# Performance work log

Measured on AMD Instinct MI355X. Metric: run time of the kernel, lower is better.

Reference implementation:

```python
import jax, jax.numpy as jnp
import numpy as np

B, L, D = 32, 512, 128          # batch, seq_len, d_model (= num graph nodes N)
E, HS, DTR, U = 64, 64, 4, 32   # d_proj_E, d_proj_H (state), dt_rank, d_proj_U
R, K, DE, NH = 3, 3, 10, 4      # mamba layers, cheb order, d_e, heads
EPS = 1e-5


def _ln(x, g, b):
    m = jnp.mean(x, -1, keepdims=True)
    v = jnp.mean((x - m) ** 2, -1, keepdims=True)
    return (x - m) / jnp.sqrt(v + EPS) * g + b


def _mamba(x, in_w, conv_w, conv_b, xproj_w, dt_w, dt_b, Alog, Dp, out_w):
    b, l, _ = x.shape
    xz = x @ in_w                                  # (b,l,2E)
    xp, res = xz[..., :E], xz[..., E:]
    xc = jnp.transpose(xp, (0, 2, 1))              # (b,E,l)
    # causal depthwise conv: torch pads both sides by d_conv-1 then slices [:l]
    xc = jax.lax.conv_general_dilated(
        xc, conv_w, (1,), [(conv_w.shape[-1] - 1, 0)],
        dimension_numbers=('NCH', 'OIH', 'NCH'), feature_group_count=E)
    xc = xc + conv_b[None, :, None]
    xp = jax.nn.silu(jnp.transpose(xc, (0, 2, 1)))  # (b,l,E)
    xdbl = xp @ xproj_w                             # (b,l,DTR+2*HS)
    delta = jax.nn.softplus(xdbl[..., :DTR] @ dt_w + dt_b)        # (b,l,E)
    Bm = xdbl[..., DTR:DTR + HS]                                   # (b,l,HS)
    Cm = xdbl[..., DTR + HS:]                                      # (b,l,HS)
    A = -jnp.exp(Alog)                                             # (E,HS)
    dA = jnp.exp(delta[..., None] * A)                             # (b,l,E,HS)
    dBu = delta[..., None] * Bm[:, :, None, :] * xp[..., None]     # (b,l,E,HS)

    def step(s, t):
        dA_t, dBu_t, C_t = t
        s = dA_t * s + dBu_t
        return s, jnp.einsum('bdn,bn->bd', s, C_t)

    _, ys = jax.lax.scan(step, jnp.zeros((b, E, HS), x.dtype),
                         (jnp.swapaxes(dA, 0, 1), jnp.swapaxes(dBu, 0, 1),
                          jnp.swapaxes(Cm, 0, 1)))
    y = jnp.swapaxes(ys, 0, 1) + xp * Dp
    y = y * jax.nn.sigmoid(res)
    return y @ out_w


def _forward(x, mb_in_w, mb_conv_w, mb_conv_b, mb_xproj_w, mb_dt_w, mb_dt_b,
             mb_Alog, mb_D, mb_out_w, ln1_g, ln1_b, ln2_g, ln2_b,
             ffn_w1, ffn_b1, ffn_w2, ffn_b2,
             psi_emb, psi, W_q, W_k, attn_alpha, F_w, f_b, head_mix,
             head_w, head_b):
    # ---- bidirectional Mamba stack ----
    for i in range(R):
        f, bk = 2 * i, 2 * i + 1
        Y1 = _mamba(x, mb_in_w[f], mb_conv_w[f], mb_conv_b[f], mb_xproj_w[f],
                    mb_dt_w[f], mb_dt_b[f], mb_Alog[f], mb_D[f], mb_out_w[f])
        Y2 = jnp.flip(_mamba(jnp.flip(x, 1), mb_in_w[bk], mb_conv_w[bk],
                             mb_conv_b[bk], mb_xproj_w[bk], mb_dt_w[bk],
                             mb_dt_b[bk], mb_Alog[bk], mb_D[bk], mb_out_w[bk]), 1)
        Y3 = _ln(x + Y1 + Y2, ln1_g[i], ln1_b[i])
        Yp = jax.nn.relu(Y3 @ ffn_w1[i] + ffn_b1[i]) @ ffn_w2[i] + ffn_b2[i]
        x = _ln(Yp + Y3, ln2_g[i], ln2_b[i])
    h = jnp.transpose(x, (0, 2, 1))                # (B, N=D, L)
    # ---- MAGAC (deterministic single MC sample, eval, no edge drop) ----
    diff = psi_emb[:, None, :] - psi_emb[None, :, :]
    A_g = jax.nn.softmax(jnp.exp(-psi * jnp.sum(diff * diff, -1)), axis=1)
    Q = jnp.einsum('nd,dhm->nhm', psi_emb, W_q)
    Kt = jnp.einsum('nd,dhm->nhm', psi_emb, W_k)
    attn = jax.nn.softmax(jnp.einsum('nhd,mhd->hnm', Q, Kt)
                          / jnp.sqrt(jnp.asarray(DE, x.dtype)), axis=-1)
    alpha = jax.nn.sigmoid(attn_alpha)
    A_effs = alpha * A_g[None] + (1.0 - alpha) * attn   # (H,N,N)
    mix = jax.nn.softmax(head_mix)
    I = jnp.eye(D, dtype=x.dtype)
    out = jnp.zeros((x.shape[0], D), x.dtype)
    for hh in range(NH):
        A = A_effs[hh]
        sup = [I, A]
        for _ in range(2, K + 1):
            sup.append(2.0 * A @ sup[-1] - sup[-2])
        S = jnp.stack(sup, 0)                             # (K+1,N,N)
        Wf = jnp.einsum('nd,dkl->nkl', psi_emb, F_w[hh])  # (N,K+1,L)
        bf = psi_emb @ f_b[hh]                            # (N,)
        out_h = jnp.einsum('knm,bml,nkl->bn', S, h, Wf) + bf
        out = out + mix[hh] * out_h
    log_var = jnp.zeros_like(out)
    pred = out @ head_w + head_b                          # (B,1)
    return pred, log_var


def setup_inputs() -> dict:
    key = jax.random.key(0)
    ks = iter(jax.random.split(key, 40))
    nrm = lambda shp, s=0.05: (jax.random.normal(next(ks), shp, jnp.float32) * s)
    M = 2 * R
    base_Alog = jnp.log(jnp.arange(1, HS + 1, dtype=jnp.float32))
    inp = {
        'x': jax.random.normal(next(ks), (B, L, D), jnp.float32),
        'mb_in_w': nrm((M, D, 2 * E)),
        'mb_conv_w': nrm((M, E, 1, 3), 0.2),
        'mb_conv_b': jnp.zeros((M, E), jnp.float32),
        'mb_xproj_w': nrm((M, E, DTR + 2 * HS)),
        'mb_dt_w': nrm((M, DTR, E), 0.2),
        'mb_dt_b': jnp.zeros((M, E), jnp.float32),
        'mb_Alog': jnp.tile(base_Alog[None, None, :], (M, E, 1)),
        'mb_D': jnp.ones((M, E), jnp.float32),
        'mb_out_w': nrm((M, E, D)),
        'ln1_g': jnp.ones((R, D), jnp.float32),
        'ln1_b': jnp.zeros((R, D), jnp.float32),
        'ln2_g': jnp.ones((R, D), jnp.float32),
        'ln2_b': jnp.zeros((R, D), jnp.float32),
        'ffn_w1': nrm((R, D, U)),
        'ffn_b1': jnp.zeros((R, U), jnp.float32),
        'ffn_w2': nrm((R, U, D)),
        'ffn_b2': jnp.zeros((R, D), jnp.float32),
        'psi_emb': jax.random.normal(next(ks), (D, DE), jnp.float32),
        'psi': jnp.asarray(1.0, jnp.float32),
        'W_q': jax.random.normal(next(ks), (DE, NH, DE), jnp.float32),
        'W_k': jax.random.normal(next(ks), (DE, NH, DE), jnp.float32),
        'attn_alpha': jnp.asarray(0.5, jnp.float32),
        'F_w': nrm((NH, DE, K + 1, L), 0.05),
        'f_b': nrm((NH, DE), 1.0),
        'head_mix': jnp.ones((NH,), jnp.float32),
        'head_w': nrm((D, 1)),
        'head_b': jnp.zeros((1,), jnp.float32),
    }
    return inp


def reference(x, mb_in_w, mb_conv_w, mb_conv_b, mb_xproj_w, mb_dt_w, mb_dt_b,
              mb_Alog, mb_D, mb_out_w, ln1_g, ln1_b, ln2_g, ln2_b,
              ffn_w1, ffn_b1, ffn_w2, ffn_b2,
              psi_emb, psi, W_q, W_k, attn_alpha, F_w, f_b, head_mix,
              head_w, head_b):
    return _forward(x, mb_in_w, mb_conv_w, mb_conv_b, mb_xproj_w, mb_dt_w,
                    mb_dt_b, mb_Alog, mb_D, mb_out_w, ln1_g, ln1_b, ln2_g,
                    ln2_b, ffn_w1, ffn_b1, ffn_w2, ffn_b2, psi_emb, psi,
                    W_q, W_k, attn_alpha, F_w, f_b, head_mix, head_w, head_b)
```

## Files before the change

### kernel.cpp

```cpp
#include <hip/hip_runtime.h>
#include <hip/hip_bf16.h>


#define B_ 32
#define L_ 512
#define D_ 128
#define E_ 64
#define HS_ 64

#define OFF_X     0u
#define OFF_XZF   2097152u
#define OFF_XZB   4194304u
#define OFF_XPF   6291456u
#define OFF_XPB   7340032u
#define OFF_PKF   8388608u
#define OFF_PKB   10485760u
#define OFF_XBCF  12582912u
#define OFF_XBCB  14680064u
#define OFF_YSF   16777216u
#define OFF_YSB   17825792u
#define OFF_V     2097152u
#define OFF_WFT   10485760u
#define OFF_STT   11534336u
#define OFF_AEFF  11796480u
#define OFF_PART  12582912u
#define OFF_RED1  16777216u

__device__ __forceinline__ float sigf(float x) { return 1.f / (1.f + __expf(-x)); }
__device__ __forceinline__ unsigned int bf16r(float x) {
    unsigned int u = __float_as_uint(x);
    return (u + 0x7fffu + ((u >> 16) & 1u)) >> 16;
}

__global__ __launch_bounds__(256) void gemm_in2_kernel(
    const float* __restrict__ X, const float* __restrict__ WF, const float* __restrict__ WB,
    float* __restrict__ xzF, float* __restrict__ xzB)
{
    __shared__ float sxT[128][36];
    __shared__ float sw[2][16][128];
    const int tid = threadIdx.x;
    const int r0 = blockIdx.x * 32;
    for (int q = tid; q < 1024; q += 256) {
        const int r = q >> 5, k4 = q & 31;
        const float4 v = *(const float4*)&X[(size_t)(r0 + r) * 128 + k4 * 4];
        sxT[k4 * 4 + 0][r] = v.x; sxT[k4 * 4 + 1][r] = v.y;
        sxT[k4 * 4 + 2][r] = v.z; sxT[k4 * 4 + 3][r] = v.w;
    }
    const int wv = tid >> 6, lane = tid & 63;
    const int d = wv >> 1, ch = wv & 1;
    const int r4 = lane >> 4, c16 = lane & 15;
    float4 acc[8];
#pragma unroll
    for (int j = 0; j < 8; ++j) acc[j] = float4{0.f, 0.f, 0.f, 0.f};
    for (int ko = 0; ko < 128; ko += 16) {
        __syncthreads();
        for (int q = tid; q < 1024; q += 256) {
            const int dd = q >> 9, kk = (q >> 5) & 15, c4 = q & 31;
            *(float4*)&sw[dd][kk][c4 * 4] =
                *(const float4*)&((dd ? WB : WF)[(ko + kk) * 128 + c4 * 4]);
        }
        __syncthreads();
#pragma unroll
        for (int kk = 0; kk < 16; ++kk) {
            const float4 w4 = *(const float4*)&sw[d][kk][ch * 64 + c16 * 4];
            const float4 xa = *(const float4*)&sxT[ko + kk][r4 * 8];
            const float4 xb = *(const float4*)&sxT[ko + kk][r4 * 8 + 4];
            const float xs[8] = {xa.x, xa.y, xa.z, xa.w, xb.x, xb.y, xb.z, xb.w};
#pragma unroll
            for (int j = 0; j < 8; ++j) {
                acc[j].x = fmaf(xs[j], w4.x, acc[j].x);
                acc[j].y = fmaf(xs[j], w4.y, acc[j].y);
                acc[j].z = fmaf(xs[j], w4.z, acc[j].z);
                acc[j].w = fmaf(xs[j], w4.w, acc[j].w);
            }
        }
    }
    float* xz = d ? xzB : xzF;
#pragma unroll
    for (int j = 0; j < 8; ++j) {
        *(float4*)&xz[(r0 + r4 * 8 + j) * 128 + ch * 64 + c16 * 4] = acc[j];
    }
}

__global__ __launch_bounds__(256) void prep4_kernel(
    const float* __restrict__ xzF_, const float* __restrict__ xzB_,
    const float* __restrict__ conv_w, const float* __restrict__ conv_b,
    const float* __restrict__ xproj_w, const float* __restrict__ dt_w,
    const float* __restrict__ dt_b, int layer,
    float* __restrict__ xpF_, float* __restrict__ xpB_,
    unsigned int* __restrict__ xbcF_, unsigned int* __restrict__ xbcB_,
    float* __restrict__ pkF_, float* __restrict__ pkB_)
{
    __shared__ float sW[8448];
    __shared__ float sxp4[4][64][4];
    __shared__ float sdl4[4][4][4];
    const int tid = threadIdx.x, wv = tid >> 6, lane = tid & 63;
    const int dir = (int)(blockIdx.x >= 1024);
    const int r0 = (blockIdx.x & 1023) * 16;
    const int b = r0 >> 9;
    const int m = layer * 2 + dir;
    const float* Wg = xproj_w + m * 8448;
    for (int q = tid; q < 2112; q += 256) ((float4*)sW)[q] = ((const float4*)Wg)[q];
    const float* xz = dir ? xzB_ : xzF_;
    float* xp  = dir ? xpB_  : xpF_;
    unsigned int* xbc = dir ? xbcB_ : xbcF_;
    float* pkx = dir ? pkB_  : pkF_;
    const float* cw = conv_w + m * 192 + lane * 3;
    const float cw0 = cw[0], cw1 = cw[1], cw2 = cw[2];
    const float cb  = conv_b[m * 64 + lane];
    const float dtb = dt_b[m * 64 + lane];
    const float* dwp = dt_w + m * 256;
    const float dw0 = dwp[lane], dw1 = dwp[64 + lane], dw2 = dwp[128 + lane], dw3 = dwp[192 + lane];
    float uu[4];
#pragma unroll
    for (int it = 0; it < 4; ++it) {
        const int row = r0 + wv * 4 + it;
        const int l = row & 511;
        const int l1 = dir ? l + 1 : l - 1;
        const int l2 = dir ? l + 2 : l - 2;
        float acc = cb;
        const float x0 = xz[(size_t)row * 128 + lane];
        const float x1 = (l1 >= 0 && l1 < 512) ? xz[(size_t)(b * 512 + l1) * 128 + lane] : 0.f;
        const float x2 = (l2 >= 0 && l2 < 512) ? xz[(size_t)(b * 512 + l2) * 128 + lane] : 0.f;
        acc += cw0 * x2 + cw1 * x1 + cw2 * x0;
        const float u = acc * sigf(acc);
        xp[row * 64 + lane] = u;
        uu[it] = u;
    }
    *(float4*)&sxp4[wv][lane][0] = float4{uu[0], uu[1], uu[2], uu[3]};
    __syncthreads();
    const int jdt = lane & 3;
    float aB[4] = {0.f, 0.f, 0.f, 0.f};
    float aC[4] = {0.f, 0.f, 0.f, 0.f};
    float adt[4] = {0.f, 0.f, 0.f, 0.f};
#pragma unroll 4
    for (int k = 0; k < 64; ++k) {
        const float wB = sW[k * 132 + 4 + lane];
        const float wC = sW[k * 132 + 68 + lane];
        const float wd = sW[k * 132 + jdt];
        const float4 xv = *(const float4*)&sxp4[wv][k][0];
        aB[0] = fmaf(xv.x, wB, aB[0]); aC[0] = fmaf(xv.x, wC, aC[0]); adt[0] = fmaf(xv.x, wd, adt[0]);
        aB[1] = fmaf(xv.y, wB, aB[1]); aC[1] = fmaf(xv.y, wC, aC[1]); adt[1] = fmaf(xv.y, wd, adt[1]);
        aB[2] = fmaf(xv.z, wB, aB[2]); aC[2] = fmaf(xv.z, wC, aC[2]); adt[2] = fmaf(xv.z, wd, adt[2]);
        aB[3] = fmaf(xv.w, wB, aB[3]); aC[3] = fmaf(xv.w, wC, aC[3]); adt[3] = fmaf(xv.w, wd, adt[3]);
    }
#pragma unroll
    for (int it = 0; it < 4; ++it) {
        const int row = r0 + wv * 4 + it;
        xbc[row * 64 + lane] = (bf16r(aC[it]) << 16) | bf16r(aB[it]);
        if (lane < 4) sdl4[wv][it][lane] = adt[it];
    }
#pragma unroll
    for (int it = 0; it < 4; ++it) {
        const int row = r0 + wv * 4 + it;
        float dpre = fmaf(sdl4[wv][it][0], dw0, dtb);
        dpre = fmaf(sdl4[wv][it][1], dw1, dpre);
        dpre = fmaf(sdl4[wv][it][2], dw2, dpre);
        dpre = fmaf(sdl4[wv][it][3], dw3, dpre);
        const float dlt = (dpre > 20.f) ? dpre : log1pf(__expf(dpre));
        ((float2*)pkx)[row * 64 + lane] = float2{dlt, dlt * uu[it]};
    }
}

__global__ __launch_bounds__(256, 4) void scan8_kernel(
    const unsigned int* __restrict__ xbcF, const unsigned int* __restrict__ xbcB,
    const float* __restrict__ pkF, const float* __restrict__ pkB,
    const float* __restrict__ AlogF, const float* __restrict__ AlogB,
    float* __restrict__ ysF, float* __restrict__ ysB)
{
    __shared__ unsigned int sbc[2][1024];
    __shared__ float spk[2][4][16][2];
    __shared__ float ytile[4][16][68];
    const int tid = threadIdx.x, wv = tid >> 6, lane = tid & 63;
    const int bx = blockIdx.x;
    const int db = bx & 63;
    const int dir = db >> 5;
    const int b   = db & 31;
    const int e0  = (bx >> 6) * 4;
    const int e   = e0 + wv;
    const unsigned int* xbc = dir ? xbcB : xbcF;
    const float* pk  = dir ? pkB  : pkF;
    const float* Aw  = dir ? AlogB : AlogF;
    float* ys = dir ? ysB : ysF;
    const float a2 = -__expf(Aw[e * 64 + lane]) * 1.4426950408889634f;
    float s = 0.f;
    float* yrow = ys + (size_t)(b * 64 + e) * 512;

    const int psl = tid & 15, pw_ = tid >> 4;

#define STG_LOAD(RS)                                                              \
    {                                                                             \
        nb = *(const uint4*)(xbc + (size_t)(RS) * 64 + tid * 4);                  \
        if (tid < 64)                                                             \
            npp = *(const float2*)(pk + (size_t)((RS) + psl) * 128 + (e0 + pw_) * 2); \
    }
#define STG_WRITE(BUF)                                                            \
    {                                                                             \
        *(uint4*)(&sbc[BUF][tid * 4]) = nb;                                       \
        if (tid < 64) *(float2*)(&spk[BUF][pw_][psl][0]) = npp;                   \
    }

#define SCAN16(REV)                                                               \
    {                                                                             \
        const unsigned int* bc = &sbc[cur][0];                                    \
        const float* pq = &spk[cur][wv][0][0];                                    \
        _Pragma("unroll")                                                         \
        for (int j = 0; j < 8; ++j) {                                             \
            const int pj = (REV) ? 7 - j : j;                                     \
            const float4 pk4 = *(const float4*)(pq + pj * 4);                     \
            const int sA = (REV) ? 15 - 2 * j : 2 * j;                            \
            const int sB = (REV) ? 14 - 2 * j : 2 * j + 1;                        \
            const float dlA = (REV) ? pk4.z : pk4.x;                              \
            const float duA = (REV) ? pk4.w : pk4.y;                              \
            const float dlB = (REV) ? pk4.x : pk4.z;                              \
            const float duB = (REV) ? pk4.y : pk4.w;                              \
            const unsigned int bA = bc[sA * 64 + lane];                           \
            const float BnA = __uint_as_float(bA << 16);                          \
            const float CnA = __uint_as_float(bA & 0xffff0000u);                  \
            s = fmaf(__builtin_amdgcn_exp2f(dlA * a2), s, duA * BnA);             \
            ytile[wv][sA][lane] = s * CnA;                                        \
            const unsigned int bB = bc[sB * 64 + lane];                           \
            const float BnB = __uint_as_float(bB << 16);                          \
            const float CnB = __uint_as_float(bB & 0xffff0000u);                  \
            s = fmaf(__builtin_amdgcn_exp2f(dlB * a2), s, duB * BnB);             \
            ytile[wv][sB][lane] = s * CnB;                                        \
        }                                                                         \
    }

    {
        uint4 nb; float2 npp;
        const int rs0 = b * 512 + (dir ? 496 : 0);
        STG_LOAD(rs0);
        STG_WRITE(0);
    }
    __syncthreads();

    int cur = 0;
    const int rr = lane & 15, sg = lane >> 4;
    for (int t = 0; t < 32; ++t) {
        uint4 nb; float2 npp;
        const bool more = (t + 1) < 32;
        if (more) {
            const int rs = b * 512 + (dir ? (496 - (t + 1) * 16) : ((t + 1) * 16));
            STG_LOAD(rs);
        }
        if (dir == 0) { SCAN16(0) } else { SCAN16(1) }
        {
            const float* yt = &ytile[wv][rr][sg * 16];
            const float4 A0 = *(const float4*)yt;
            const float4 A1 = *(const float4*)(yt + 4);
            const float4 A2 = *(const float4*)(yt + 8);
            const float4 A3 = *(const float4*)(yt + 12);
            float p = ((A0.x + A0.y) + (A0.z + A0.w)) + ((A1.x + A1.y) + (A1.z + A1.w))
                    + ((A2.x + A2.y) + (A2.z + A2.w)) + ((A3.x + A3.y) + (A3.z + A3.w));
            p += __shfl_xor(p, 16);
            p += __shfl_xor(p, 32);
            if (lane < 16) {
                const int lg = dir ? (496 + rr - t * 16) : (t * 16 + rr);
                yrow[lg] = p;
            }
        }
        if (more) STG_WRITE(cur ^ 1);
        __syncthreads();
        cur ^= 1;
    }
#undef STG_LOAD
#undef STG_WRITE
#undef SCAN16
}

__global__ __launch_bounds__(256, 4) void opfn3_kernel(
    const float* __restrict__ ysF, const float* __restrict__ ysB,
    const float* __restrict__ xpF, const float* __restrict__ xpB,
    const float* __restrict__ xzF, const float* __restrict__ xzB,
    const float* __restrict__ Dp, int layer,
    const float* __restrict__ Xc, const float* __restrict__ out_w,
    const float* __restrict__ W1, const float* __restrict__ b1,
    const float* __restrict__ W2, const float* __restrict__ b2,
    const float* __restrict__ g1, const float* __restrict__ bb1,
    const float* __restrict__ g2, const float* __restrict__ bb2,
    float* __restrict__ xout,
    const float* __restrict__ WFn, const float* __restrict__ WBn,
    float* __restrict__ xzFo, float* __restrict__ xzBo)
{
    __shared__ float smem[9216];
    float* syy = smem;
    float* sw  = smem + 4096;
    float* sh  = smem + 8192;
    const int tid = threadIdx.x;
    const int r0 = blockIdx.x * 32;
    const int b = r0 >> 9, l0 = r0 & 511;
    const int wv = tid >> 6, lane = tid & 63;
    const float* WFp = out_w + (layer * 2) * 8192;
    const float* WBp = out_w + (layer * 2 + 1) * 8192;

    for (int q = tid; q < 1024; q += 256) {
        const int d = q >> 9, ee = (q >> 3) & 63, rq = q & 7;
        const float* ysp = d ? ysB : ysF;
        const float4 v = *(const float4*)&ysp[(size_t)(b * 64 + ee) * 512 + l0 + rq * 4];
        const float dv = Dp[(layer * 2 + d) * 64 + ee];
        const float* xpp = d ? xpB : xpF;
        const float* xzp = d ? xzB : xzF;
        const float vv[4] = {v.x, v.y, v.z, v.w};
#pragma unroll
        for (int j = 0; j < 4; ++j) {
            const int r = rq * 4 + j;
            const int row = r0 + r;
            const float u   = xpp[(size_t)row * 64 + ee];
            const float res = xzp[(size_t)row * 128 + 64 + ee];
            syy[r * 128 + d * 64 + ee] = (vv[j] + u * dv) * sigf(res);
        }
    }
    __syncthreads();

    float acc[8][2];
#pragma unroll
    for (int r = 0; r < 8; ++r) { acc[r][0] = 0.f; acc[r][1] = 0.f; }
#define OPSTEP8(COMP, J)                                                          \
        {                                                                         \
            const float w0 = sw[(kk + (J)) * 128 + lane];                         \
            const float w1 = sw[(kk + (J)) * 128 + lane + 64];                    \
            acc[0][0] = fmaf(y40.COMP, w0, acc[0][0]); acc[0][1] = fmaf(y40.COMP, w1, acc[0][1]); \
            acc[1][0] = fmaf(y41.COMP, w0, acc[1][0]); acc[1][1] = fmaf(y41.COMP, w1, acc[1][1]); \
            acc[2][0] = fmaf(y42.COMP, w0, acc[2][0]); acc[2][1] = fmaf(y42.COMP, w1, acc[2][1]); \
            acc[3][0] = fmaf(y43.COMP, w0, acc[3][0]); acc[3][1] = fmaf(y43.COMP, w1, acc[3][1]); \
            acc[4][0] = fmaf(y44.COMP, w0, acc[4][0]); acc[4][1] = fmaf(y44.COMP, w1, acc[4][1]); \
            acc[5][0] = fmaf(y45.COMP, w0, acc[5][0]); acc[5][1] = fmaf(y45.COMP, w1, acc[5][1]); \
            acc[6][0] = fmaf(y46.COMP, w0, acc[6][0]); acc[6][1] = fmaf(y46.COMP, w1, acc[6][1]); \
            acc[7][0] = fmaf(y47.COMP, w0, acc[7][0]); acc[7][1] = fmaf(y47.COMP, w1, acc[7][1]); \
        }
#define GEMM_CHUNK8(SRC, KO)                                                      \
    _Pragma("unroll")                                                             \
    for (int kk = 0; kk < 32; kk += 4) {                                          \
        const float4 y40 = *(const float4*)&(SRC)[(wv * 8 + 0) * 128 + (KO) + kk];\
        const float4 y41 = *(const float4*)&(SRC)[(wv * 8 + 1) * 128 + (KO) + kk];\
        const float4 y42 = *(const float4*)&(SRC)[(wv * 8 + 2) * 128 + (KO) + kk];\
        const float4 y43 = *(const float4*)&(SRC)[(wv * 8 + 3) * 128 + (KO) + kk];\
        const float4 y44 = *(const float4*)&(SRC)[(wv * 8 + 4) * 128 + (KO) + kk];\
        const float4 y45 = *(const float4*)&(SRC)[(wv * 8 + 5) * 128 + (KO) + kk];\
        const float4 y46 = *(const float4*)&(SRC)[(wv * 8 + 6) * 128 + (KO) + kk];\
        const float4 y47 = *(const float4*)&(SRC)[(wv * 8 + 7) * 128 + (KO) + kk];\
        OPSTEP8(x, 0) OPSTEP8(y, 1) OPSTEP8(z, 2) OPSTEP8(w, 3)                  \
    }
    for (int koi = 0; koi < 4; ++koi) {
        if (koi) __syncthreads();
        for (int q = tid; q < 1024; q += 256) {
            const int kk = q >> 5, c4 = q & 31;
            const int kg = koi * 32 + kk;
            *(float4*)&sw[kk * 128 + c4 * 4] = (kg < 64)
                ? *(const float4*)&WFp[kg * 128 + c4 * 4]
                : *(const float4*)&WBp[(kg - 64) * 128 + c4 * 4];
        }
        __syncthreads();
        GEMM_CHUNK8(syy, koi * 32);
    }
    __syncthreads();
    for (int q = tid; q < 1024; q += 256) ((float4*)sw)[q] = ((const float4*)W1)[q];
#pragma unroll
    for (int r = 0; r < 8; ++r) {
        const int rl = wv * 8 + r;
        const int row = r0 + rl;
        float v0 = acc[r][0] + Xc[(size_t)row * 128 + lane];
        float v1 = acc[r][1] + Xc[(size_t)row * 128 + lane + 64];
        float sum = v0 + v1, sq = v0 * v0 + v1 * v1;
#pragma unroll
        for (int o = 32; o >= 1; o >>= 1) { sum += __shfl_xor(sum, o); sq += __shfl_xor(sq, o); }
        const float mean = sum * (1.f / 128.f);
        const float var = sq * (1.f / 128.f) - mean * mean;
        const float rs = rsqrtf(var + 1e-5f);
        syy[rl * 128 + lane]      = (v0 - mean) * rs * g1[lane] + bb1[lane];
        syy[rl * 128 + lane + 64] = (v1 - mean) * rs * g1[lane + 64] + bb1[lane + 64];
    }
    __syncthreads();
    {
        const int r = tid >> 3, ug = (tid & 7) * 4;
        float h0 = b1[ug], h1 = b1[ug + 1], h2 = b1[ug + 2], h3 = b1[ug + 3];
#pragma unroll 8
        for (int k = 0; k < 128; ++k) {
            const float xv = syy[r * 128 + k];
            h0 = fmaf(xv, sw[k * 32 + ug], h0);
            h1 = fmaf(xv, sw[k * 32 + ug + 1], h1);
            h2 = fmaf(xv, sw[k * 32 + ug + 2], h2);
            h3 = fmaf(xv, sw[k * 32 + ug + 3], h3);
        }
        sh[r * 32 + ug]     = fmaxf(h0, 0.f);
        sh[r * 32 + ug + 1] = fmaxf(h1, 0.f);
        sh[r * 32 + ug + 2] = fmaxf(h2, 0.f);
        sh[r * 32 + ug + 3] = fmaxf(h3, 0.f);
    }
    __syncthreads();
    for (int q = tid; q < 1024; q += 256) ((float4*)sw)[q] = ((const float4*)W2)[q];
    __syncthreads();
    float xr[8][2];
#pragma unroll
    for (int r = 0; r < 8; ++r) {
        const int rl = wv * 8 + r;
        float a0 = b2[lane], a1 = b2[lane + 64];
#pragma unroll 8
        for (int k = 0; k < 32; ++k) {
            const float hv = sh[rl * 32 + k];
            a0 = fmaf(hv, sw[k * 128 + lane], a0);
            a1 = fmaf(hv, sw[k * 128 + lane + 64], a1);
        }
        const float v0 = a0 + syy[rl * 128 + lane];
        const float v1 = a1 + syy[rl * 128 + lane + 64];
        float sum = v0 + v1, sq = v0 * v0 + v1 * v1;
#pragma unroll
        for (int o = 32; o >= 1; o >>= 1) { sum += __shfl_xor(sum, o); sq += __shfl_xor(sq, o); }
        const float mean = sum * (1.f / 128.f);
        const float var = sq * (1.f / 128.f) - mean * mean;
        const float rs = rsqrtf(var + 1e-5f);
        const int row = r0 + rl;
        const float o0 = (v0 - mean) * rs * g2[lane] + bb2[lane];
        const float o1 = (v1 - mean) * rs * g2[lane + 64] + bb2[lane + 64];
        xout[(size_t)row * 128 + lane]      = o0;
        xout[(size_t)row * 128 + lane + 64] = o1;
        xr[r][0] = o0; xr[r][1] = o1;
    }
    if (WFn == nullptr) return;
    __syncthreads();
    float* sxr = syy;
#pragma unroll
    for (int r = 0; r < 8; ++r) {
        sxr[(wv * 8 + r) * 128 + lane]      = xr[r][0];
        sxr[(wv * 8 + r) * 128 + lane + 64] = xr[r][1];
    }
    for (int c = 0; c < 8; ++c) {
        const int dd = c >> 2, ko = (c & 3) * 32;
        const float* Wn = dd ? WBn : WFn;
        for (int q = tid; q < 1024; q += 256) {
            const int kk = q >> 5, c4 = q & 31;
            *(float4*)&sw[kk * 128 + c4 * 4] = *(const float4*)&Wn[(ko + kk) * 128 + c4 * 4];
        }
        __syncthreads();
        if ((c & 3) == 0) {
#pragma unroll
            for (int r = 0; r < 8; ++r) { acc[r][0] = 0.f; acc[r][1] = 0.f; }
        }
        GEMM_CHUNK8(sxr, ko);
        if ((c & 3) == 3) {
            float* xzo = dd ? xzBo : xzFo;
#pragma unroll
            for (int r = 0; r < 8; ++r) {
                const int row = r0 + wv * 8 + r;
                xzo[(size_t)row * 128 + lane]      = acc[r][0];
                xzo[(size_t)row * 128 + lane + 64] = acc[r][1];
            }
        }
        __syncthreads();
    }
#undef OPSTEP8
#undef GEMM_CHUNK8
}

__global__ __launch_bounds__(256) void head_wfqk_kernel(
    const float* __restrict__ psi, const float* __restrict__ F_w, float* __restrict__ WfT,
    const float* __restrict__ psis, const float* __restrict__ W_q, const float* __restrict__ W_k,
    const float* __restrict__ attn_a,
    float* __restrict__ Aeff, float* __restrict__ StT)
{
    __shared__ float sQ[2][10];
    __shared__ float red[2][128];
    if (blockIdx.x < 4096) {
        const int idx = blockIdx.x * 256 + threadIdx.x;
        const int n = idx & 127, l = (idx >> 7) & 511, k = (idx >> 16) & 3, h = idx >> 18;
        float acc = 0.f;
#pragma unroll
        for (int d = 0; d < 10; ++d)
            acc = fmaf(psi[n * 10 + d], F_w[((h * 10 + d) * 4 + k) * 512 + l], acc);
        WfT[idx] = acc;
        return;
    }
    const int q = blockIdx.x - 4096;
    const int half = threadIdx.x >> 7, mcol = threadIdx.x & 127;
    const int unit = q * 2 + half;
    const int h = unit >> 7, n = unit & 127;
    float Kreg[10];
#pragma unroll
    for (int d = 0; d < 10; ++d) Kreg[d] = 0.f;
#pragma unroll
    for (int d0 = 0; d0 < 10; ++d0) {
        const float pv = psi[mcol * 10 + d0];
#pragma unroll
        for (int d = 0; d < 10; ++d) Kreg[d] = fmaf(pv, W_k[(d0 * 4 + h) * 10 + d], Kreg[d]);
    }
    if (mcol < 10) {
        float qd = 0.f;
        for (int d0 = 0; d0 < 10; ++d0)
            qd = fmaf(psi[n * 10 + d0], W_q[(d0 * 4 + h) * 10 + mcol], qd);
        sQ[half][mcol] = qd;
    }
    __syncthreads();
    float d2 = 0.f;
#pragma unroll
    for (int d = 0; d < 10; ++d) { const float df = psi[n * 10 + d] - psi[mcol * 10 + d]; d2 = fmaf(df, df, d2); }
    const float gv = __expf(-psis[0] * d2);
    float qv = 0.f;
#pragma unroll
    for (int d = 0; d < 10; ++d) qv = fmaf(sQ[half][d], Kreg[d], qv);
    qv *= 0.3162277660168379332f;
    float* rd = red[half];
    float r;
    rd[mcol] = gv; __syncthreads();
    for (int s = 64; s >= 1; s >>= 1) { if (mcol < s) rd[mcol] = fmaxf(rd[mcol], rd[mcol + s]); __syncthreads(); }
    r = rd[0]; __syncthreads();
    const float eg = __expf(gv - r);
    rd[mcol] = eg; __syncthreads();
    for (int s = 64; s >= 1; s >>= 1) { if (mcol < s) rd[mcol] += rd[mcol + s]; __syncthreads(); }
    const float gsum = rd[0]; __syncthreads();
    rd[mcol] = qv; __syncthreads();
    for (int s = 64; s >= 1; s >>= 1) { if (mcol < s) rd[mcol] = fmaxf(rd[mcol], rd[mcol + s]); __syncthreads(); }
    r = rd[0]; __syncthreads();
    const float eq = __expf(qv - r);
    rd[mcol] = eq; __syncthreads();
    for (int s = 64; s >= 1; s >>= 1) { if (mcol < s) rd[mcol] += rd[mcol + s]; __syncthreads(); }
    const float qsum = rd[0];
    const float al = sigf(attn_a[0]);
    const float aeff = al * (eg / gsum) + (1.f - al) * (eq / qsum);
    Aeff[h * 16384 + n * 128 + mcol] = aeff;
    StT[((h * 4 + 1) * 128 + mcol) * 128 + n] = aeff;
    StT[((h * 4 + 0) * 128 + mcol) * 128 + n] = (mcol == n) ? 1.f : 0.f;
}

__global__ __launch_bounds__(256) void head_cheb_kernel(
    const float* __restrict__ Aeff, float* __restrict__ StT, int kk)
{
    const int h = blockIdx.x >> 6;
    const int m0 = ((blockIdx.x & 63) << 1) + (threadIdx.x >> 7);
    const int n = threadIdx.x & 127;
    const float* Ar = Aeff + h * 16384 + n * 128;
    const float* Sp = StT + ((h * 4 + kk - 1) * 128 + m0) * 128;
    float acc = 0.f;
#pragma unroll 8
    for (int p = 0; p < 128; ++p) acc = fmaf(Ar[p], Sp[p], acc);
    const float s2 = StT[((h * 4 + kk - 2) * 128 + m0) * 128 + n];
    StT[((h * 4 + kk) * 128 + m0) * 128 + n] = 2.f * acc - s2;
}

__global__ __launch_bounds__(256) void head_v4_kernel(
    const float* __restrict__ StT, const float* __restrict__ WfT, const float* __restrict__ hmix,
    float* __restrict__ V)
{
    const float m0 = hmix[0], m1 = hmix[1], m2 = hmix[2], m3 = hmix[3];
    const float mxx = fmaxf(fmaxf(m0, m1), fmaxf(m2, m3));
    const float e0 = __expf(m0 - mxx), e1 = __expf(m1 - mxx), e2 = __expf(m2 - mxx), e3 = __expf(m3 - mxx);
    const float inv = 1.f / (e0 + e1 + e2 + e3);
    const float mixv[4] = {e0 * inv, e1 * inv, e2 * inv, e3 * inv};
    const int tid = threadIdx.x;
    const int lt = blockIdx.x & 63, mm = blockIdx.x >> 6;
    const int n4 = tid & 31, mh = tid >> 5;
    const int m = mm * 8 + mh;
    const int l0 = lt * 8, n0 = n4 * 4;
    float4 sv[16];
#pragma unroll
    for (int h = 0; h < 4; ++h) {
        const float mx = mixv[h];
#pragma unroll
        for (int k = 0; k < 4; ++k) {
            const float4 v = *(const float4*)&StT[(size_t)((h * 4 + k) * 128 + m) * 128 + n0];
            sv[h * 4 + k] = float4{v.x * mx, v.y * mx, v.z * mx, v.w * mx};
        }
    }
#pragma unroll
    for (int j = 0; j < 8; ++j) {
        const int l = l0 + j;
        float4 acc = {0.f, 0.f, 0.f, 0.f};
#pragma unroll
        for (int hk = 0; hk < 16; ++hk) {
            const float4 w = *(const float4*)&WfT[(size_t)(hk * 512 + l) * 128 + n0];
            acc.x = fmaf(sv[hk].x, w.x, acc.x);
            acc.y = fmaf(sv[hk].y, w.y, acc.y);
            acc.z = fmaf(sv[hk].z, w.z, acc.z);
            acc.w = fmaf(sv[hk].w, w.w, acc.w);
        }
        *(float4*)&V[(size_t)(l * 128 + m) * 128 + n0] = acc;
    }
}

__global__ __launch_bounds__(256) void head_ctr_kernel(
    const float* __restrict__ Xf, const float* __restrict__ V, float* __restrict__ partial)
{
    __shared__ float sx[32][128];
    const int l = blockIdx.x, tid = threadIdx.x;
    const int n = tid & 127, mh = tid >> 7;
    for (int q = tid; q < 1024; q += 256) {
        const int b = q >> 5, m4 = q & 31;
        *(float4*)&sx[b][m4 * 4] = *(const float4*)&Xf[(size_t)(b * 512 + l) * 128 + m4 * 4];
    }
    __syncthreads();
    float acc[32];
#pragma unroll
    for (int b = 0; b < 32; ++b) acc[b] = 0.f;
    const float* vp = V + (size_t)(l * 128 + mh * 64) * 128 + n;
    for (int mm = 0; mm < 64; ++mm) {
        const float v = vp[(size_t)mm * 128];
        const int m = mh * 64 + mm;
#pragma unroll
        for (int b = 0; b < 32; ++b) acc[b] = fmaf(sx[b][m], v, acc[b]);
    }
#pragma unroll
    for (int b = 0; b < 32; ++b)
        partial[(size_t)((l * 2 + mh) * 32 + b) * 128 + n] = acc[b];
}

__global__ __launch_bounds__(128) void head_red_kernel(
    const float* __restrict__ partial, float* __restrict__ red1)
{
    const int b = blockIdx.x >> 5, cs = blockIdx.x & 31, n = threadIdx.x;
    const float* p = partial + ((size_t)(cs * 32) * 32 + b) * 128 + n;
    float s = 0.f;
#pragma unroll 8
    for (int c = 0; c < 32; ++c) s += p[(size_t)c * 4096];
    red1[(b * 32 + cs) * 128 + n] = s;
}

__global__ __launch_bounds__(128) void head_out_kernel(
    const float* __restrict__ red1, const float* __restrict__ psi,
    const float* __restrict__ f_b, const float* __restrict__ hmix,
    const float* __restrict__ head_w, const float* __restrict__ head_b, float* __restrict__ out)
{
    __shared__ float red[128];
    const int b = blockIdx.x, n = threadIdx.x;
    const float m0 = hmix[0], m1 = hmix[1], m2 = hmix[2], m3 = hmix[3];
    const float mxx = fmaxf(fmaxf(m0, m1), fmaxf(m2, m3));
    const float e0 = __expf(m0 - mxx), e1 = __expf(m1 - mxx), e2 = __expf(m2 - mxx), e3 = __expf(m3 - mxx);
    const float inv = 1.f / (e0 + e1 + e2 + e3);
    const float mixv[4] = {e0 * inv, e1 * inv, e2 * inv, e3 * inv};
    float s = 0.f;
#pragma unroll
    for (int h = 0; h < 4; ++h) {
        float t = 0.f;
#pragma unroll
        for (int d = 0; d < 10; ++d) t = fmaf(psi[n * 10 + d], f_b[h * 10 + d], t);
        s = fmaf(mixv[h], t, s);
    }
#pragma unroll 8
    for (int cs = 0; cs < 32; ++cs) s += red1[(b * 32 + cs) * 128 + n];
    red[n] = s * head_w[n];
    __syncthreads();
    for (int st = 64; st >= 1; st >>= 1) { if (n < st) red[n] += red[n + st]; __syncthreads(); }
    if (n == 0) out[b] = red[0] + head_b[0];
    out[32 + b * 128 + n] = 0.f;
}

extern "C" void kernel_launch(void* const* d_in, const int* in_sizes, int n_in,
                              void* d_out, int out_size, void* d_ws, size_t ws_size,
                              hipStream_t stream) {
    const float* x_in    = (const float*)d_in[0];
    const float* in_w    = (const float*)d_in[1];
    const float* conv_w  = (const float*)d_in[2];
    const float* conv_b  = (const float*)d_in[3];
    const float* xproj_w = (const float*)d_in[4];
    const float* dt_w    = (const float*)d_in[5];
    const float* dt_b    = (const float*)d_in[6];
    const float* Alog    = (const float*)d_in[7];
    const float* Dp      = (const float*)d_in[8];
    const float* out_w   = (const float*)d_in[9];
    const float* ln1_g   = (const float*)d_in[10];
    const float* ln1_b   = (const float*)d_in[11];
    const float* ln2_g   = (const float*)d_in[12];
    const float* ln2_b   = (const float*)d_in[13];
    const float* ffn_w1  = (const float*)d_in[14];
    const float* ffn_b1  = (const float*)d_in[15];
    const float* ffn_w2  = (const float*)d_in[16];
    const float* ffn_b2  = (const float*)d_in[17];
    const float* psi_emb = (const float*)d_in[18];
    const float* psi_s   = (const float*)d_in[19];
    const float* W_q     = (const float*)d_in[20];
    const float* W_k     = (const float*)d_in[21];
    const float* attn_a  = (const float*)d_in[22];
    const float* F_w     = (const float*)d_in[23];
    const float* f_b     = (const float*)d_in[24];
    const float* hmix    = (const float*)d_in[25];
    const float* head_w  = (const float*)d_in[26];
    const float* head_b  = (const float*)d_in[27];
    float* ws = (float*)d_ws;
    float* outp = (float*)d_out;

    gemm_in2_kernel<<<512, 256, 0, stream>>>(
        x_in, in_w, in_w + 16384, ws + OFF_XZF, ws + OFF_XZB);
    for (int i = 0; i < 3; ++i) {
        const float* xcur = (i == 0) ? x_in : (ws + OFF_X);
        const int mF = 2 * i, mB = 2 * i + 1;
        prep4_kernel<<<2048, 256, 0, stream>>>(
            ws + OFF_XZF, ws + OFF_XZB, conv_w, conv_b, xproj_w, dt_w, dt_b, i,
            ws + OFF_XPF, ws + OFF_XPB,
            (unsigned int*)(ws + OFF_XBCF), (unsigned int*)(ws + OFF_XBCB),
            ws + OFF_PKF, ws + OFF_PKB);
        scan8_kernel<<<1024, 256, 0, stream>>>(
            (const unsigned int*)(ws + OFF_XBCF), (const unsigned int*)(ws + OFF_XBCB),
            ws + OFF_PKF, ws + OFF_PKB,
            Alog + mF * 4096, Alog + mB * 4096, ws + OFF_YSF, ws + OFF_YSB);
        const float* WFn = (i < 2) ? (in_w + (2 * i + 2) * 16384) : nullptr;
        const float* WBn = (i < 2) ? (in_w + (2 * i + 3) * 16384) : nullptr;
        opfn3_kernel<<<512, 256, 0, stream>>>(
            ws + OFF_YSF, ws + OFF_YSB, ws + OFF_XPF, ws + OFF_XPB, ws + OFF_XZF, ws + OFF_XZB,
            Dp, i, xcur, out_w,
            ffn_w1 + i * 4096, ffn_b1 + i * 32, ffn_w2 + i * 4096, ffn_b2 + i * 128,
            ln1_g + i * 128, ln1_b + i * 128, ln2_g + i * 128, ln2_b + i * 128,
            ws + OFF_X, WFn, WBn, ws + OFF_XZF, ws + OFF_XZB);
    }
    head_wfqk_kernel<<<4352, 256, 0, stream>>>(
        psi_emb, F_w, ws + OFF_WFT, psi_s, W_q, W_k, attn_a,
        ws + OFF_AEFF, ws + OFF_STT);
    head_cheb_kernel<<<256, 256, 0, stream>>>(ws + OFF_AEFF, ws + OFF_STT, 2);
    head_cheb_kernel<<<256, 256, 0, stream>>>(ws + OFF_AEFF, ws + OFF_STT, 3);
    head_v4_kernel<<<1024, 256, 0, stream>>>(ws + OFF_STT, ws + OFF_WFT, hmix, ws + OFF_V);
    head_ctr_kernel<<<512, 256, 0, stream>>>(ws + OFF_X, ws + OFF_V, ws + OFF_PART);
    head_red_kernel<<<1024, 128, 0, stream>>>(ws + OFF_PART, ws + OFF_RED1);
    head_out_kernel<<<32, 128, 0, stream>>>(
        ws + OFF_RED1, psi_emb, f_b, hmix, head_w, head_b, outp);
}
```

Measured before the change: 507.8 us.

## Fold graph-head precompute into Mamba layer kernels as extra blocks

```diff
diff --git a/kernel.cpp b/kernel.cpp
--- a/kernel.cpp
+++ b/kernel.cpp
@@ -16,13 +16,13 @@
 #define OFF_PKF   8388608u
 #define OFF_PKB   10485760u
 #define OFF_XBCF  12582912u
+#define OFF_WFT   13631488u
 #define OFF_XBCB  14680064u
+#define OFF_STT   15728640u
+#define OFF_AEFF  15990784u
 #define OFF_YSF   16777216u
 #define OFF_YSB   17825792u
 #define OFF_V     2097152u
-#define OFF_WFT   10485760u
-#define OFF_STT   11534336u
-#define OFF_AEFF  11796480u
 #define OFF_PART  12582912u
 #define OFF_RED1  16777216u
 
@@ -30,6 +30,89 @@
 __device__ __forceinline__ unsigned int bf16r(float x) {
     unsigned int u = __float_as_uint(x);
     return (u + 0x7fffu + ((u >> 16) & 1u)) >> 16;
+}
+
+__device__ void role_wf(int bx0, int tid, const float* __restrict__ psi,
+                        const float* __restrict__ F_w, float* __restrict__ WfT)
+{
+    const int idx = bx0 * 256 + tid;
+    const int n = idx & 127, l = (idx >> 7) & 511, k = (idx >> 16) & 3, h = idx >> 18;
+    float acc = 0.f;
+#pragma unroll
+    for (int d = 0; d < 10; ++d)
+        acc = fmaf(psi[n * 10 + d], F_w[((h * 10 + d) * 4 + k) * 512 + l], acc);
+    WfT[idx] = acc;
+}
+
+__device__ void role_qkaeff(int bx0, int tid, const float* __restrict__ psi,
+                            const float* __restrict__ psis, const float* __restrict__ W_q,
+                            const float* __restrict__ W_k, const float* __restrict__ attn_a,
+                            float* __restrict__ Aeff, float* __restrict__ StT,
+                            float* sQ2 , float* red2 )
+{
+    const int half = tid >> 7, mcol = tid & 127;
+    const int unit = bx0 * 2 + half;
+    const int h = unit >> 7, n = unit & 127;
+    float Kreg[10];
+#pragma unroll
+    for (int d = 0; d < 10; ++d) Kreg[d] = 0.f;
+#pragma unroll
+    for (int d0 = 0; d0 < 10; ++d0) {
+        const float pv = psi[mcol * 10 + d0];
+#pragma unroll
+        for (int d = 0; d < 10; ++d) Kreg[d] = fmaf(pv, W_k[(d0 * 4 + h) * 10 + d], Kreg[d]);
+    }
+    if (mcol < 10) {
+        float qd = 0.f;
+        for (int d0 = 0; d0 < 10; ++d0)
+            qd = fmaf(psi[n * 10 + d0], W_q[(d0 * 4 + h) * 10 + mcol], qd);
+        sQ2[half * 16 + mcol] = qd;
+    }
+    __syncthreads();
+    float d2 = 0.f;
+#pragma unroll
+    for (int d = 0; d < 10; ++d) { const float df = psi[n * 10 + d] - psi[mcol * 10 + d]; d2 = fmaf(df, df, d2); }
+    const float gv = __expf(-psis[0] * d2);
+    float qv = 0.f;
+#pragma unroll
+    for (int d = 0; d < 10; ++d) qv = fmaf(sQ2[half * 16 + d], Kreg[d], qv);
+    qv *= 0.3162277660168379332f;
+    float* rd = red2 + half * 128;
+    float r;
+    rd[mcol] = gv; __syncthreads();
+    for (int s = 64; s >= 1; s >>= 1) { if (mcol < s) rd[mcol] = fmaxf(rd[mcol], rd[mcol + s]); __syncthreads(); }
+    r = rd[0]; __syncthreads();
+    const float eg = __expf(gv - r);
+    rd[mcol] = eg; __syncthreads();
+    for (int s = 64; s >= 1; s >>= 1) { if (mcol < s) rd[mcol] += rd[mcol + s]; __syncthreads(); }
+    const float gsum = rd[0]; __syncthreads();
+    rd[mcol] = qv; __syncthreads();
+    for (int s = 64; s >= 1; s >>= 1) { if (mcol < s) rd[mcol] = fmaxf(rd[mcol], rd[mcol + s]); __syncthreads(); }
+    r = rd[0]; __syncthreads();
+    const float eq = __expf(qv - r);
+    rd[mcol] = eq; __syncthreads();
+    for (int s = 64; s >= 1; s >>= 1) { if (mcol < s) rd[mcol] += rd[mcol + s]; __syncthreads(); }
+    const float qsum = rd[0];
+    const float al = sigf(attn_a[0]);
+    const float aeff = al * (eg / gsum) + (1.f - al) * (eq / qsum);
+    Aeff[h * 16384 + n * 128 + mcol] = aeff;
+    StT[((h * 4 + 1) * 128 + mcol) * 128 + n] = aeff;
+    StT[((h * 4 + 0) * 128 + mcol) * 128 + n] = (mcol == n) ? 1.f : 0.f;
+}
+
+__device__ void role_cheb(int bx0, int tid, const float* __restrict__ Aeff,
+                          float* __restrict__ StT, int kk)
+{
+    const int h = bx0 >> 6;
+    const int m0 = ((bx0 & 63) << 1) + (tid >> 7);
+    const int n = tid & 127;
+    const float* Ar = Aeff + h * 16384 + n * 128;
+    const float* Sp = StT + ((h * 4 + kk - 1) * 128 + m0) * 128;
+    float acc = 0.f;
+#pragma unroll 8
+    for (int p = 0; p < 128; ++p) acc = fmaf(Ar[p], Sp[p], acc);
+    const float s2 = StT[((h * 4 + kk - 2) * 128 + m0) * 128 + n];
+    StT[((h * 4 + kk) * 128 + m0) * 128 + n] = 2.f * acc - s2;
 }
 
 __global__ __launch_bounds__(256) void gemm_in2_kernel(
@@ -89,12 +172,20 @@
     const float* __restrict__ dt_b, int layer,
     float* __restrict__ xpF_, float* __restrict__ xpB_,
     unsigned int* __restrict__ xbcF_, unsigned int* __restrict__ xbcB_,
-    float* __restrict__ pkF_, float* __restrict__ pkB_)
+    float* __restrict__ pkF_, float* __restrict__ pkB_,
+    const float* __restrict__ psi, const float* __restrict__ F_w, float* __restrict__ WfT,
+    const float* __restrict__ Aeff, float* __restrict__ StT)
 {
     __shared__ float sW[8448];
     __shared__ float sxp4[4][64][4];
     __shared__ float sdl4[4][4][4];
     const int tid = threadIdx.x, wv = tid >> 6, lane = tid & 63;
+    if (blockIdx.x >= 2048) {
+        const int bx0 = blockIdx.x - 2048;
+        if (layer == 0) role_wf(bx0, tid, psi, F_w, WfT);
+        else            role_cheb(bx0, tid, Aeff, StT, 3);
+        return;
+    }
     const int dir = (int)(blockIdx.x >= 1024);
     const int r0 = (blockIdx.x & 1023) * 16;
     const int b = r0 >> 9;
@@ -166,13 +257,21 @@
     const unsigned int* __restrict__ xbcF, const unsigned int* __restrict__ xbcB,
     const float* __restrict__ pkF, const float* __restrict__ pkB,
     const float* __restrict__ AlogF, const float* __restrict__ AlogB,
-    float* __restrict__ ysF, float* __restrict__ ysB)
+    float* __restrict__ ysF, float* __restrict__ ysB,
+    const float* __restrict__ psi, const float* __restrict__ psis,
+    const float* __restrict__ W_q, const float* __restrict__ W_k,
+    const float* __restrict__ attn_a, float* __restrict__ Aeff, float* __restrict__ StT)
 {
     __shared__ unsigned int sbc[2][1024];
     __shared__ float spk[2][4][16][2];
     __shared__ float ytile[4][16][68];
     const int tid = threadIdx.x, wv = tid >> 6, lane = tid & 63;
     const int bx = blockIdx.x;
+    if (bx >= 1024) {
+        role_qkaeff(bx - 1024, tid, psi, psis, W_q, W_k, attn_a, Aeff, StT,
+                    (float*)&sbc[1][0], (float*)&sbc[0][0]);
+        return;
+    }
     const int db = bx & 63;
     const int dir = db >> 5;
     const int b   = db & 31;
@@ -281,13 +380,18 @@
     const float* __restrict__ g2, const float* __restrict__ bb2,
     float* __restrict__ xout,
     const float* __restrict__ WFn, const float* __restrict__ WBn,
-    float* __restrict__ xzFo, float* __restrict__ xzBo)
+    float* __restrict__ xzFo, float* __restrict__ xzBo,
+    const float* __restrict__ Aeff, float* __restrict__ StT)
 {
     __shared__ float smem[9216];
     float* syy = smem;
     float* sw  = smem + 4096;
     float* sh  = smem + 8192;
     const int tid = threadIdx.x;
+    if (blockIdx.x >= 512) {
+        role_cheb(blockIdx.x - 512, tid, Aeff, StT, 2);
+        return;
+    }
     const int r0 = blockIdx.x * 32;
     const int b = r0 >> 9, l0 = r0 & 511;
     const int wv = tid >> 6, lane = tid & 63;
@@ -451,90 +555,6 @@
     }
 #undef OPSTEP8
 #undef GEMM_CHUNK8
-}
-
-__global__ __launch_bounds__(256) void head_wfqk_kernel(
-    const float* __restrict__ psi, const float* __restrict__ F_w, float* __restrict__ WfT,
-    const float* __restrict__ psis, const float* __restrict__ W_q, const float* __restrict__ W_k,
-    const float* __restrict__ attn_a,
-    float* __restrict__ Aeff, float* __restrict__ StT)
-{
-    __shared__ float sQ[2][10];
-    __shared__ float red[2][128];
-    if (blockIdx.x < 4096) {
-        const int idx = blockIdx.x * 256 + threadIdx.x;
-        const int n = idx & 127, l = (idx >> 7) & 511, k = (idx >> 16) & 3, h = idx >> 18;
-        float acc = 0.f;
-#pragma unroll
-        for (int d = 0; d < 10; ++d)
-            acc = fmaf(psi[n * 10 + d], F_w[((h * 10 + d) * 4 + k) * 512 + l], acc);
-        WfT[idx] = acc;
-        return;
-    }
-    const int q = blockIdx.x - 4096;
-    const int half = threadIdx.x >> 7, mcol = threadIdx.x & 127;
-    const int unit = q * 2 + half;
-    const int h = unit >> 7, n = unit & 127;
-    float Kreg[10];
-#pragma unroll
-    for (int d = 0; d < 10; ++d) Kreg[d] = 0.f;
-#pragma unroll
-    for (int d0 = 0; d0 < 10; ++d0) {
-        const float pv = psi[mcol * 10 + d0];
-#pragma unroll
-        for (int d = 0; d < 10; ++d) Kreg[d] = fmaf(pv, W_k[(d0 * 4 + h) * 10 + d], Kreg[d]);
-    }
-    if (mcol < 10) {
-        float qd = 0.f;
-        for (int d0 = 0; d0 < 10; ++d0)
-            qd = fmaf(psi[n * 10 + d0], W_q[(d0 * 4 + h) * 10 + mcol], qd);
-        sQ[half][mcol] = qd;
-    }
-    __syncthreads();
-    float d2 = 0.f;
-#pragma unroll
-    for (int d = 0; d < 10; ++d) { const float df = psi[n * 10 + d] - psi[mcol * 10 + d]; d2 = fmaf(df, df, d2); }
-    const float gv = __expf(-psis[0] * d2);
-    float qv = 0.f;
-#pragma unroll
-    for (int d = 0; d < 10; ++d) qv = fmaf(sQ[half][d], Kreg[d], qv);
-    qv *= 0.3162277660168379332f;
-    float* rd = red[half];
-    float r;
-    rd[mcol] = gv; __syncthreads();
-    for (int s = 64; s >= 1; s >>= 1) { if (mcol < s) rd[mcol] = fmaxf(rd[mcol], rd[mcol + s]); __syncthreads(); }
-    r = rd[0]; __syncthreads();
-    const float eg = __expf(gv - r);
-    rd[mcol] = eg; __syncthreads();
-    for (int s = 64; s >= 1; s >>= 1) { if (mcol < s) rd[mcol] += rd[mcol + s]; __syncthreads(); }
-    const float gsum = rd[0]; __syncthreads();
-    rd[mcol] = qv; __syncthreads();
-    for (int s = 64; s >= 1; s >>= 1) { if (mcol < s) rd[mcol] = fmaxf(rd[mcol], rd[mcol + s]); __syncthreads(); }
-    r = rd[0]; __syncthreads();
-    const float eq = __expf(qv - r);
-    rd[mcol] = eq; __syncthreads();
-    for (int s = 64; s >= 1; s >>= 1) { if (mcol < s) rd[mcol] += rd[mcol + s]; __syncthreads(); }
-    const float qsum = rd[0];
-    const float al = sigf(attn_a[0]);
-    const float aeff = al * (eg / gsum) + (1.f - al) * (eq / qsum);
-    Aeff[h * 16384 + n * 128 + mcol] = aeff;
-    StT[((h * 4 + 1) * 128 + mcol) * 128 + n] = aeff;
-    StT[((h * 4 + 0) * 128 + mcol) * 128 + n] = (mcol == n) ? 1.f : 0.f;
-}
-
-__global__ __launch_bounds__(256) void head_cheb_kernel(
-    const float* __restrict__ Aeff, float* __restrict__ StT, int kk)
-{
-    const int h = blockIdx.x >> 6;
-    const int m0 = ((blockIdx.x & 63) << 1) + (threadIdx.x >> 7);
-    const int n = threadIdx.x & 127;
-    const float* Ar = Aeff + h * 16384 + n * 128;
-    const float* Sp = StT + ((h * 4 + kk - 1) * 128 + m0) * 128;
-    float acc = 0.f;
-#pragma unroll 8
-    for (int p = 0; p < 128; ++p) acc = fmaf(Ar[p], Sp[p], acc);
-    const float s2 = StT[((h * 4 + kk - 2) * 128 + m0) * 128 + n];
-    StT[((h * 4 + kk) * 128 + m0) * 128 + n] = 2.f * acc - s2;
 }
 
 __global__ __launch_bounds__(256) void head_v4_kernel(
@@ -682,29 +702,30 @@
     for (int i = 0; i < 3; ++i) {
         const float* xcur = (i == 0) ? x_in : (ws + OFF_X);
         const int mF = 2 * i, mB = 2 * i + 1;
-        prep4_kernel<<<2048, 256, 0, stream>>>(
+        const int prep_grid = (i == 0) ? 6144 : (i == 1) ? 2304 : 2048;
+        prep4_kernel<<<prep_grid, 256, 0, stream>>>(
             ws + OFF_XZF, ws + OFF_XZB, conv_w, conv_b, xproj_w, dt_w, dt_b, i,
             ws + OFF_XPF, ws + OFF_XPB,
             (unsigned int*)(ws + OFF_XBCF), (unsigned int*)(ws + OFF_XBCB),
-            ws + OFF_PKF, ws + OFF_PKB);
-        scan8_kernel<<<1024, 256, 0, stream>>>(
+            ws + OFF_PKF, ws + OFF_PKB,
+            psi_emb, F_w, ws + OFF_WFT, ws + OFF_AEFF, ws + OFF_STT);
+        const int scan_grid = (i == 0) ? 1280 : 1024;
+        scan8_kernel<<<scan_grid, 256, 0, stream>>>(
             (const unsigned int*)(ws + OFF_XBCF), (const unsigned int*)(ws + OFF_XBCB),
             ws + OFF_PKF, ws + OFF_PKB,
-            Alog + mF * 4096, Alog + mB * 4096, ws + OFF_YSF, ws + OFF_YSB);
+            Alog + mF * 4096, Alog + mB * 4096, ws + OFF_YSF, ws + OFF_YSB,
+            psi_emb, psi_s, W_q, W_k, attn_a, ws + OFF_AEFF, ws + OFF_STT);
         const float* WFn = (i < 2) ? (in_w + (2 * i + 2) * 16384) : nullptr;
         const float* WBn = (i < 2) ? (in_w + (2 * i + 3) * 16384) : nullptr;
-        opfn3_kernel<<<512, 256, 0, stream>>>(
+        const int opfn_grid = (i == 0) ? 768 : 512;
+        opfn3_kernel<<<opfn_grid, 256, 0, stream>>>(
             ws + OFF_YSF, ws + OFF_YSB, ws + OFF_XPF, ws + OFF_XPB, ws + OFF_XZF, ws + OFF_XZB,
             Dp, i, xcur, out_w,
             ffn_w1 + i * 4096, ffn_b1 + i * 32, ffn_w2 + i * 4096, ffn_b2 + i * 128,
             ln1_g + i * 128, ln1_b + i * 128, ln2_g + i * 128, ln2_b + i * 128,
-            ws + OFF_X, WFn, WBn, ws + OFF_XZF, ws + OFF_XZB);
-    }
-    head_wfqk_kernel<<<4352, 256, 0, stream>>>(
-        psi_emb, F_w, ws + OFF_WFT, psi_s, W_q, W_k, attn_a,
-        ws + OFF_AEFF, ws + OFF_STT);
-    head_cheb_kernel<<<256, 256, 0, stream>>>(ws + OFF_AEFF, ws + OFF_STT, 2);
-    head_cheb_kernel<<<256, 256, 0, stream>>>(ws + OFF_AEFF, ws + OFF_STT, 3);
+            ws + OFF_X, WFn, WBn, ws + OFF_XZF, ws + OFF_XZB,
+            ws + OFF_AEFF, ws + OFF_STT);
+    }
     head_v4_kernel<<<1024, 256, 0, stream>>>(ws + OFF_STT, ws + OFF_WFT, hmix, ws + OFF_V);
     head_ctr_kernel<<<512, 256, 0, stream>>>(ws + OFF_X, ws + OFF_V, ws + OFF_PART);
     head_red_kernel<<<1024, 128, 0, stream>>>(ws + OFF_PART, ws + OFF_RED1);
```

Measured after the change: 479.3 us. 1.06x faster.
